# Optimization experiments

Measured on AMD Instinct MI355X. Metric: run time of the kernel, lower is better.

Reference implementation:

```python
import jax, jax.numpy as jnp
import numpy as np

N_NODES = 100000
N_EDGES = 1600000
IN_DIM = 128
OUT_DIM = 64
EDGE_DIM = 8


def setup_inputs() -> dict:
    key = jax.random.key(0)
    ks = jax.random.split(key, 7)
    h = jax.random.normal(ks[0], (N_NODES, IN_DIM), dtype=jnp.float32)
    edge_index = jax.random.randint(ks[1], (2, N_EDGES), 0, N_NODES, dtype=jnp.int64)
    edge_attr = jax.random.normal(ks[2], (N_EDGES, EDGE_DIM), dtype=jnp.float32)
    w_w = jax.random.normal(ks[3], (IN_DIM, OUT_DIM), dtype=jnp.float32) * (1.0 / np.sqrt(IN_DIM))
    w_b = jax.random.normal(ks[4], (OUT_DIM,), dtype=jnp.float32) * 0.01
    a_w = jax.random.normal(ks[5], (2 * OUT_DIM + EDGE_DIM, 1), dtype=jnp.float32) * 0.1
    a_b = jax.random.normal(ks[6], (1,), dtype=jnp.float32) * 0.01
    return {"h": h, "edge_index": edge_index, "edge_attr": edge_attr,
            "w_w": w_w, "w_b": w_b, "a_w": a_w, "a_b": a_b}


def reference(h, edge_index, edge_attr, w_w, w_b, a_w, a_b):
    n = h.shape[0]
    d = w_w.shape[1]
    wh = h @ w_w + w_b                              # [N, out_dim]
    row, col = edge_index[0], edge_index[1]
    # a([wh[row], wh[col], edge_attr]) == wh[row]@a1 + wh[col]@a2 + edge_attr@a3 + b
    a1, a2, a3 = a_w[:d], a_w[d:2 * d], a_w[2 * d:]
    s_row = wh @ a1                                 # [N, 1] per-node attention terms
    s_col = wh @ a2                                 # [N, 1]
    e = jax.nn.leaky_relu(s_row[row] + s_col[col] + edge_attr @ a3 + a_b)  # [E, 1]
    # segment softmax over edges grouped by destination `row`
    max_e = jax.ops.segment_max(e, row, num_segments=n)     # [N, 1]
    alpha = jnp.exp(e - max_e[row])                          # [E, 1]
    out = jax.ops.segment_sum(alpha * wh[col], row, num_segments=n)  # [N, out_dim]
    norm = jax.ops.segment_sum(alpha, row, num_segments=n)           # [N, 1]
    return out / (norm + 1e-8)
```

## Files before the change

kernel.cpp:

```cpp
#include <hip/hip_runtime.h>
#include <hip/hip_fp16.h>

#define IN_DIM 128
#define OUT_DIM 64
#define RPB 512
#define MAXB 200
#define EPB 2048

typedef __attribute__((ext_vector_type(8))) _Float16 half8;
typedef __attribute__((ext_vector_type(4))) float f32x4;

__global__ __launch_bounds__(256) void k_wh(
    const float* __restrict__ h, const float* __restrict__ w_w,
    const float* __restrict__ w_b, const float* __restrict__ a_w,
    __half* __restrict__ wh, float* __restrict__ s_row,
    float* __restrict__ s_col, int n_nodes) {
  __shared__ _Float16 wf[4 * 4 * 64 * 8];
  for (int idx = threadIdx.x; idx < IN_DIM * OUT_DIM; idx += 256) {
    int k = idx >> 6, c = idx & 63;
    int mt = c >> 4;
    int kt = k >> 5;
    int l = (((k >> 3) & 3) << 4) | (c & 15);
    int j = k & 7;
    wf[(((mt << 2) | kt) << 9) | (l << 3) | j] = (_Float16)w_w[idx];
  }
  __syncthreads();

  const int lane = threadIdx.x & 63;
  const int wv = threadIdx.x >> 6;

  half8 A[4][4];
#pragma unroll
  for (int mt = 0; mt < 4; ++mt)
#pragma unroll
    for (int kt = 0; kt < 4; ++kt)
      A[mt][kt] =
          *(const half8*)&wf[(((mt << 2) | kt) << 9) | (lane << 3)];

  const int cbase = (lane >> 4) << 2;
  f32x4 bq[4], a1q[4], a2q[4];
#pragma unroll
  for (int mt = 0; mt < 4; ++mt) {
    bq[mt] = *(const f32x4*)&w_b[mt * 16 + cbase];
    a1q[mt] = *(const f32x4*)&a_w[mt * 16 + cbase];
    a2q[mt] = *(const f32x4*)&a_w[OUT_DIM + mt * 16 + cbase];
  }

  const int ntiles = (n_nodes + 15) >> 4;
  const int tstride = gridDim.x << 2;
  for (int t = blockIdx.x * 4 + wv; t < ntiles; t += tstride) {
    const int n0 = t << 4;
    const int node = n0 + (lane & 15);
    const int nodec = node < n_nodes ? node : n_nodes - 1;
    const float4* hv =
        (const float4*)(h + (size_t)nodec * IN_DIM + ((lane >> 4) << 3));
    float4 p[8];
#pragma unroll
    for (int kt = 0; kt < 4; ++kt) {
      p[2 * kt] = hv[kt * 8];
      p[2 * kt + 1] = hv[kt * 8 + 1];
    }
    f32x4 C[4];
#pragma unroll
    for (int mt = 0; mt < 4; ++mt) C[mt] = (f32x4){0.f, 0.f, 0.f, 0.f};
#pragma unroll
    for (int kt = 0; kt < 4; ++kt) {
      const float4 u = p[2 * kt], v = p[2 * kt + 1];
      half8 B;
      B[0] = (_Float16)u.x; B[1] = (_Float16)u.y;
      B[2] = (_Float16)u.z; B[3] = (_Float16)u.w;
      B[4] = (_Float16)v.x; B[5] = (_Float16)v.y;
      B[6] = (_Float16)v.z; B[7] = (_Float16)v.w;
#pragma unroll
      for (int mt = 0; mt < 4; ++mt)
        C[mt] = __builtin_amdgcn_mfma_f32_16x16x32_f16(A[mt][kt], B, C[mt],
                                                       0, 0, 0);
    }
    float sr = 0.f, sc = 0.f;
    uint2 q[4];
#pragma unroll
    for (int mt = 0; mt < 4; ++mt) {
      f32x4 d = C[mt] + bq[mt];
      sr += d[0] * a1q[mt][0] + d[1] * a1q[mt][1] + d[2] * a1q[mt][2] +
            d[3] * a1q[mt][3];
      sc += d[0] * a2q[mt][0] + d[1] * a2q[mt][1] + d[2] * a2q[mt][2] +
            d[3] * a2q[mt][3];
      __half2 lo = __floats2half2_rn(d[0], d[1]);
      __half2 hi = __floats2half2_rn(d[2], d[3]);
      q[mt].x = *(unsigned int*)&lo;
      q[mt].y = *(unsigned int*)&hi;
    }
    if (node < n_nodes) {
      uint2* wrow = (uint2*)(wh + (size_t)node * OUT_DIM + cbase);
      wrow[0] = q[0];
      wrow[4] = q[1];
      wrow[8] = q[2];
      wrow[12] = q[3];
    }
    sr += __shfl_xor(sr, 16, 64);
    sr += __shfl_xor(sr, 32, 64);
    sc += __shfl_xor(sc, 16, 64);
    sc += __shfl_xor(sc, 32, 64);
    if (lane < 16 && node < n_nodes) {
      s_row[node] = sr;
      s_col[node] = sc;
    }
  }
}

__global__ __launch_bounds__(512) void k_pre(
    const int* __restrict__ ei, int* __restrict__ blockhist, int nedges) {
  __shared__ int hist[MAXB];
  for (int b = threadIdx.x; b < MAXB; b += 512) hist[b] = 0;
  __syncthreads();
  const int e0 = blockIdx.x * EPB;
  if (e0 + EPB <= nedges) {
    const int e = e0 + threadIdx.x;
    int r0 = ei[e];
    int r1 = ei[e + 512];
    int r2 = ei[e + 1024];
    int r3 = ei[e + 1536];
    atomicAdd(&hist[r0 >> 9], 1);
    atomicAdd(&hist[r1 >> 9], 1);
    atomicAdd(&hist[r2 >> 9], 1);
    atomicAdd(&hist[r3 >> 9], 1);
  } else {
#pragma unroll
    for (int r = 0; r < EPB / 512; ++r) {
      int e = e0 + r * 512 + threadIdx.x;
      if (e < nedges) atomicAdd(&hist[ei[e] >> 9], 1);
    }
  }
  __syncthreads();
  for (int b = threadIdx.x; b < MAXB; b += 512)
    blockhist[blockIdx.x * MAXB + b] = hist[b];
}

__global__ __launch_bounds__(512) void k_scanA(
    const int* __restrict__ blockhist, int* __restrict__ boff,
    int* __restrict__ cnt, int nbl) {
  __shared__ int sd[512];
  const int b = blockIdx.x, t = threadIdx.x;
  int i0 = 2 * t, i1 = 2 * t + 1;
  int v0 = (i0 < nbl) ? ((blockhist[i0 * MAXB + b] + 7) & ~7) : 0;
  int v1 = (i1 < nbl) ? ((blockhist[i1 * MAXB + b] + 7) & ~7) : 0;
  int ts = v0 + v1;
  sd[t] = ts;
  __syncthreads();
  for (int off = 1; off < 512; off <<= 1) {
    int x = (t >= off) ? sd[t - off] : 0;
    __syncthreads();
    sd[t] += x;
    __syncthreads();
  }
  int excl = sd[t] - ts;
  if (i0 < nbl) boff[i0 * MAXB + b] = excl;
  if (i1 < nbl) boff[i1 * MAXB + b] = excl + v0;
  if (t == 511) cnt[b] = sd[511];
}

__global__ __launch_bounds__(256) void k_scanB(
    const int* __restrict__ cnt, int* __restrict__ bbase, int nb) {
  __shared__ int sd[256];
  int t = threadIdx.x;
  int pc = (t < nb) ? ((cnt[t] + 15) & ~15) : 0;
  sd[t] = pc;
  __syncthreads();
  for (int off = 1; off < 256; off <<= 1) {
    int x = (t >= off) ? sd[t - off] : 0;
    __syncthreads();
    sd[t] += x;
    __syncthreads();
  }
  if (t < nb) bbase[t] = sd[t] - pc;
}

__global__ __launch_bounds__(512) void k_fill(
    const int* __restrict__ ei, const float* __restrict__ edge_attr,
    const float* __restrict__ a_w, const float* __restrict__ a_b,
    const float* __restrict__ s_row, const float* __restrict__ s_col,
    const int* __restrict__ boff, const int* __restrict__ bbase,
    int2* __restrict__ entA, int nedges, int nb) {
  __shared__ int cur[MAXB];
  for (int b = threadIdx.x; b < MAXB; b += 512)
    cur[b] = (b < nb) ? bbase[b] + boff[blockIdx.x * MAXB + b] : 0;
  float aw0 = a_w[128], aw1 = a_w[129], aw2 = a_w[130], aw3 = a_w[131];
  float aw4 = a_w[132], aw5 = a_w[133], aw6 = a_w[134], aw7 = a_w[135];
  float ab = a_b[0];
  __syncthreads();
  const int e0 = blockIdx.x * EPB;
  if (e0 + EPB <= nedges) {
    const int e = e0 + threadIdx.x;
    int row[4], col[4];
#pragma unroll
    for (int r = 0; r < 4; ++r) {
      row[r] = ei[e + r * 512];
      col[r] = ei[nedges + e + r * 512];
    }
    float4 u[4], v[4];
#pragma unroll
    for (int r = 0; r < 4; ++r) {
      const float4* ea = (const float4*)(edge_attr + (size_t)(e + r * 512) * 8);
      u[r] = ea[0];
      v[r] = ea[1];
    }
    float sr[4], sc[4];
#pragma unroll
    for (int r = 0; r < 4; ++r) {
      sr[r] = s_row[row[r]];
      sc[r] = s_col[col[r]];
    }
#pragma unroll
    for (int r = 0; r < 4; ++r) {
      float s = sr[r] + sc[r] + ab;
      s += u[r].x * aw0 + u[r].y * aw1 + u[r].z * aw2 + u[r].w * aw3;
      s += v[r].x * aw4 + v[r].y * aw5 + v[r].z * aw6 + v[r].w * aw7;
      float ev = (s > 0.f) ? s : 0.01f * s;
      float alpha = __expf(ev);
      int pos = atomicAdd(&cur[row[r] >> 9], 1);
      entA[pos] =
          make_int2(((row[r] & 511) << 17) | col[r], __float_as_int(alpha));
    }
  } else {
    for (int r = 0; r < EPB / 512; ++r) {
      int e = e0 + r * 512 + threadIdx.x;
      if (e < nedges) {
        int row = ei[e];
        int col = ei[nedges + e];
        const float4* ea = (const float4*)(edge_attr + (size_t)e * 8);
        float4 u = ea[0], v = ea[1];
        float s = s_row[row] + s_col[col] + ab;
        s += u.x * aw0 + u.y * aw1 + u.z * aw2 + u.w * aw3;
        s += v.x * aw4 + v.y * aw5 + v.z * aw6 + v.w * aw7;
        float ev = (s > 0.f) ? s : 0.01f * s;
        float alpha = __expf(ev);
        int pos = atomicAdd(&cur[row >> 9], 1);
        entA[pos] = make_int2(((row & 511) << 17) | col, __float_as_int(alpha));
      }
    }
  }
  __syncthreads();
  for (int b = threadIdx.x; b < nb; b += 512) {
    int c = cur[b], end = (c + 7) & ~7;
    for (int k = c; k < end; ++k) entA[k] = make_int2(-1, 0);
  }
}

__global__ __launch_bounds__(512) void k_sortb(
    const int2* __restrict__ entA, int2* __restrict__ entB,
    const int* __restrict__ cnt, const int* __restrict__ bbase,
    int* __restrict__ nodeoffs, int* __restrict__ nodecnt, int n_nodes) {
  __shared__ int hist[RPB];
  __shared__ int loffs[RPB];
  __shared__ int cur[RPB];
  const int b = blockIdx.x, t = threadIdx.x;
  const int c = cnt[b];
  const int base = bbase[b];
  const int row0 = b << 9;
  hist[t] = 0;
  __syncthreads();
  for (int i = t; i < c; i += 512) {
    int x = entA[base + i].x;
    if (x >= 0) atomicAdd(&hist[x >> 17], 1);
  }
  __syncthreads();
  int hh = hist[t];
  loffs[t] = hh;
  __syncthreads();
  for (int off = 1; off < 512; off <<= 1) {
    int x = (t >= off) ? loffs[t - off] : 0;
    __syncthreads();
    loffs[t] += x;
    __syncthreads();
  }
  int excl = loffs[t] - hh;
  cur[t] = excl;
  int node = row0 + t;
  if (node < n_nodes) {
    nodeoffs[node] = base + excl;
    nodecnt[node] = hh;
  }
  __syncthreads();
  for (int i = t; i < c; i += 512) {
    int2 p = entA[base + i];
    if (p.x >= 0) {
      int pos = atomicAdd(&cur[p.x >> 17], 1);
      entB[base + pos] = p;
    }
  }
}

__global__ __launch_bounds__(256) void k_agg(
    const int* __restrict__ nodeoffs, const int* __restrict__ nodecnt,
    const int2* __restrict__ ent, const __half* __restrict__ wh,
    float* __restrict__ out, int n_nodes) {
  int v = blockIdx.x * 4 + (threadIdx.x >> 6);
  if (v >= n_nodes) return;
  const int lane = threadIdx.x & 63;
  const int slot = lane >> 3, sub = lane & 7;
  const int start = __builtin_amdgcn_readfirstlane(nodeoffs[v]);
  const int deg = __builtin_amdgcn_readfirstlane(nodecnt[v]);
  const uint4* whq = (const uint4*)wh;
  float acc[8] = {0.f, 0.f, 0.f, 0.f, 0.f, 0.f, 0.f, 0.f};
  float l = 0.f;
  for (int base = 0; base < deg; base += 16) {
    const int i0 = base + slot, i1 = base + 8 + slot;
    const bool g0 = i0 < deg, g1 = i1 < deg;
    int2 p0 = make_int2(0, 0), p1 = make_int2(0, 0);
    if (g0) p0 = ent[start + i0];
    if (g1) p1 = ent[start + i1];
    uint4 q0 = make_uint4(0, 0, 0, 0), q1 = make_uint4(0, 0, 0, 0);
    if (g0) q0 = whq[(size_t)(p0.x & 0x1FFFF) * 8 + sub];
    if (g1) q1 = whq[(size_t)(p1.x & 0x1FFFF) * 8 + sub];
    if (g0) {
      float a = __int_as_float(p0.y);
      float2 f0 = __half22float2(*(__half2*)&q0.x);
      float2 f1 = __half22float2(*(__half2*)&q0.y);
      float2 f2 = __half22float2(*(__half2*)&q0.z);
      float2 f3 = __half22float2(*(__half2*)&q0.w);
      acc[0] = fmaf(a, f0.x, acc[0]); acc[1] = fmaf(a, f0.y, acc[1]);
      acc[2] = fmaf(a, f1.x, acc[2]); acc[3] = fmaf(a, f1.y, acc[3]);
      acc[4] = fmaf(a, f2.x, acc[4]); acc[5] = fmaf(a, f2.y, acc[5]);
      acc[6] = fmaf(a, f3.x, acc[6]); acc[7] = fmaf(a, f3.y, acc[7]);
      if (sub == 0) l += a;
    }
    if (g1) {
      float a = __int_as_float(p1.y);
      float2 f0 = __half22float2(*(__half2*)&q1.x);
      float2 f1 = __half22float2(*(__half2*)&q1.y);
      float2 f2 = __half22float2(*(__half2*)&q1.z);
      float2 f3 = __half22float2(*(__half2*)&q1.w);
      acc[0] = fmaf(a, f0.x, acc[0]); acc[1] = fmaf(a, f0.y, acc[1]);
      acc[2] = fmaf(a, f1.x, acc[2]); acc[3] = fmaf(a, f1.y, acc[3]);
      acc[4] = fmaf(a, f2.x, acc[4]); acc[5] = fmaf(a, f2.y, acc[5]);
      acc[6] = fmaf(a, f3.x, acc[6]); acc[7] = fmaf(a, f3.y, acc[7]);
      if (sub == 0) l += a;
    }
  }
#pragma unroll
  for (int c = 0; c < 8; ++c) {
    acc[c] += __shfl_xor(acc[c], 8, 64);
    acc[c] += __shfl_xor(acc[c], 16, 64);
    acc[c] += __shfl_xor(acc[c], 32, 64);
  }
  l += __shfl_xor(l, 8, 64);
  l += __shfl_xor(l, 16, 64);
  l += __shfl_xor(l, 32, 64);
  float lt = __shfl(l, 0, 64);
  if (slot == 0) {
    float inv = 1.0f / (lt + 1e-8f);
    float4 o0 = make_float4(acc[0] * inv, acc[1] * inv, acc[2] * inv,
                            acc[3] * inv);
    float4 o1 = make_float4(acc[4] * inv, acc[5] * inv, acc[6] * inv,
                            acc[7] * inv);
    float4* orow = (float4*)out + (size_t)v * 16 + sub * 2;
    orow[0] = o0;
    orow[1] = o1;
  }
}

extern "C" void kernel_launch(void* const* d_in, const int* in_sizes, int n_in,
                              void* d_out, int out_size, void* d_ws, size_t ws_size,
                              hipStream_t stream) {
  const float* h         = (const float*)d_in[0];
  const int*   ei        = (const int*)d_in[1];
  const float* edge_attr = (const float*)d_in[2];
  const float* w_w       = (const float*)d_in[3];
  const float* w_b       = (const float*)d_in[4];
  const float* a_w       = (const float*)d_in[5];
  const float* a_b       = (const float*)d_in[6];
  const int n_nodes = in_sizes[0] / IN_DIM;
  const int nedges  = in_sizes[1] / 2;
  const int nb   = (n_nodes + RPB - 1) / RPB;
  const int nebl = (nedges + EPB - 1) / EPB;

  const size_t entcap = (size_t)nedges + (size_t)nebl * nb * 8 + (size_t)nb * 16;

  __half* wh       = (__half*)d_ws;
  int2*  entA      = (int2*)(wh + (size_t)n_nodes * OUT_DIM);
  int*   cnt       = (int*)(entA + entcap);
  int*   bbase     = cnt + MAXB;
  int*   nodeoffs  = bbase + MAXB;
  int*   nodecnt   = nodeoffs + n_nodes;
  int2*  entB      = (int2*)(nodecnt + n_nodes);
  float* s_row     = (float*)entB;
  float* s_col     = s_row + n_nodes;
  int*   blockhist = (int*)(s_col + n_nodes);
  int*   boff      = blockhist + (size_t)nebl * MAXB;

  k_wh<<<640, 256, 0, stream>>>(h, w_w, w_b, a_w, wh, s_row, s_col, n_nodes);
  k_pre<<<nebl, 512, 0, stream>>>(ei, blockhist, nedges);
  k_scanA<<<nb, 512, 0, stream>>>(blockhist, boff, cnt, nebl);
  k_scanB<<<1, 256, 0, stream>>>(cnt, bbase, nb);
  k_fill<<<nebl, 512, 0, stream>>>(ei, edge_attr, a_w, a_b, s_row, s_col,
                                   boff, bbase, entA, nedges, nb);
  k_sortb<<<nb, 512, 0, stream>>>(entA, entB, cnt, bbase, nodeoffs, nodecnt, n_nodes);
  k_agg<<<(n_nodes + 3) / 4, 256, 0, stream>>>(nodeoffs, nodecnt, entB, wh,
                                               (float*)d_out, n_nodes);
}
```

Baseline: 272.9 us.

## Build CSR via global per-node atomic histogram instead of two-level bucket sort

Replaces the block-histogram bucket partition plus per-bucket local sort with a direct CSR build: per-node degree counting via global atomics, a three-stage device prefix scan, and per-edge atomic slot allocation in the fill kernel. This removes the k_sortb pass and the bucket padding, cutting an extra read/write of the edge array. In exchange it issues millions of global atomics to random addresses and makes edge order within each node nondeterministic. Node counters are zeroed inside the projection kernel.

Measured after the change: 371.4 us. 1.36x slower.

```diff
diff --git a/kernel.cpp b/kernel.cpp
--- a/kernel.cpp
+++ b/kernel.cpp
@@ -3,8 +3,6 @@
 
 #define IN_DIM 128
 #define OUT_DIM 64
-#define RPB 512
-#define MAXB 200
 #define EPB 2048
 
 typedef __attribute__((ext_vector_type(8))) _Float16 half8;
@@ -14,7 +12,11 @@
     const float* __restrict__ h, const float* __restrict__ w_w,
     const float* __restrict__ w_b, const float* __restrict__ a_w,
     __half* __restrict__ wh, float* __restrict__ s_row,
-    float* __restrict__ s_col, int n_nodes) {
+    float* __restrict__ s_col, int* __restrict__ nodecnt, int n_nodes) {
+  {
+    int tid = blockIdx.x * 256 + threadIdx.x;
+    if (tid < n_nodes) nodecnt[tid] = 0;
+  }
   __shared__ _Float16 wf[4 * 4 * 64 * 8];
   for (int idx = threadIdx.x; idx < IN_DIM * OUT_DIM; idx += 256) {
     int k = idx >> 6, c = idx & 63;
@@ -108,11 +110,8 @@
   }
 }
 
-__global__ __launch_bounds__(512) void k_pre(
-    const int* __restrict__ ei, int* __restrict__ blockhist, int nedges) {
-  __shared__ int hist[MAXB];
-  for (int b = threadIdx.x; b < MAXB; b += 512) hist[b] = 0;
-  __syncthreads();
+__global__ __launch_bounds__(512) void k_hist(
+    const int* __restrict__ ei, int* __restrict__ nodecnt, int nedges) {
   const int e0 = blockIdx.x * EPB;
   if (e0 + EPB <= nedges) {
     const int e = e0 + threadIdx.x;
@@ -120,74 +119,69 @@
     int r1 = ei[e + 512];
     int r2 = ei[e + 1024];
     int r3 = ei[e + 1536];
-    atomicAdd(&hist[r0 >> 9], 1);
-    atomicAdd(&hist[r1 >> 9], 1);
-    atomicAdd(&hist[r2 >> 9], 1);
-    atomicAdd(&hist[r3 >> 9], 1);
+    atomicAdd(&nodecnt[r0], 1);
+    atomicAdd(&nodecnt[r1], 1);
+    atomicAdd(&nodecnt[r2], 1);
+    atomicAdd(&nodecnt[r3], 1);
   } else {
 #pragma unroll
     for (int r = 0; r < EPB / 512; ++r) {
       int e = e0 + r * 512 + threadIdx.x;
-      if (e < nedges) atomicAdd(&hist[ei[e] >> 9], 1);
-    }
-  }
+      if (e < nedges) atomicAdd(&nodecnt[ei[e]], 1);
+    }
+  }
+}
+
+__global__ __launch_bounds__(1024) void k_scan1(
+    const int* __restrict__ nodecnt, int* __restrict__ nodeoffs,
+    int* __restrict__ blocksum, int n_nodes) {
+  __shared__ int sd[1024];
+  const int t = threadIdx.x;
+  const int i = blockIdx.x * 1024 + t;
+  int v = (i < n_nodes) ? nodecnt[i] : 0;
+  sd[t] = v;
   __syncthreads();
-  for (int b = threadIdx.x; b < MAXB; b += 512)
-    blockhist[blockIdx.x * MAXB + b] = hist[b];
-}
-
-__global__ __launch_bounds__(512) void k_scanA(
-    const int* __restrict__ blockhist, int* __restrict__ boff,
-    int* __restrict__ cnt, int nbl) {
-  __shared__ int sd[512];
-  const int b = blockIdx.x, t = threadIdx.x;
-  int i0 = 2 * t, i1 = 2 * t + 1;
-  int v0 = (i0 < nbl) ? ((blockhist[i0 * MAXB + b] + 7) & ~7) : 0;
-  int v1 = (i1 < nbl) ? ((blockhist[i1 * MAXB + b] + 7) & ~7) : 0;
-  int ts = v0 + v1;
-  sd[t] = ts;
-  __syncthreads();
-  for (int off = 1; off < 512; off <<= 1) {
+  for (int off = 1; off < 1024; off <<= 1) {
     int x = (t >= off) ? sd[t - off] : 0;
     __syncthreads();
     sd[t] += x;
     __syncthreads();
   }
-  int excl = sd[t] - ts;
-  if (i0 < nbl) boff[i0 * MAXB + b] = excl;
-  if (i1 < nbl) boff[i1 * MAXB + b] = excl + v0;
-  if (t == 511) cnt[b] = sd[511];
-}
-
-__global__ __launch_bounds__(256) void k_scanB(
-    const int* __restrict__ cnt, int* __restrict__ bbase, int nb) {
-  __shared__ int sd[256];
-  int t = threadIdx.x;
-  int pc = (t < nb) ? ((cnt[t] + 15) & ~15) : 0;
-  sd[t] = pc;
+  if (i < n_nodes) nodeoffs[i] = sd[t] - v;
+  if (t == 1023) blocksum[blockIdx.x] = sd[1023];
+}
+
+__global__ __launch_bounds__(128) void k_scan2(
+    const int* __restrict__ blocksum, int* __restrict__ blockbase, int nsb) {
+  __shared__ int sd[128];
+  const int t = threadIdx.x;
+  int v = (t < nsb) ? blocksum[t] : 0;
+  sd[t] = v;
   __syncthreads();
-  for (int off = 1; off < 256; off <<= 1) {
+  for (int off = 1; off < 128; off <<= 1) {
     int x = (t >= off) ? sd[t - off] : 0;
     __syncthreads();
     sd[t] += x;
     __syncthreads();
   }
-  if (t < nb) bbase[t] = sd[t] - pc;
+  if (t < nsb) blockbase[t] = sd[t] - v;
+}
+
+__global__ __launch_bounds__(1024) void k_scan3(
+    int* __restrict__ nodeoffs, const int* __restrict__ blockbase,
+    int n_nodes) {
+  const int i = blockIdx.x * 1024 + threadIdx.x;
+  if (i < n_nodes) nodeoffs[i] += blockbase[blockIdx.x];
 }
 
 __global__ __launch_bounds__(512) void k_fill(
     const int* __restrict__ ei, const float* __restrict__ edge_attr,
     const float* __restrict__ a_w, const float* __restrict__ a_b,
     const float* __restrict__ s_row, const float* __restrict__ s_col,
-    const int* __restrict__ boff, const int* __restrict__ bbase,
-    int2* __restrict__ entA, int nedges, int nb) {
-  __shared__ int cur[MAXB];
-  for (int b = threadIdx.x; b < MAXB; b += 512)
-    cur[b] = (b < nb) ? bbase[b] + boff[blockIdx.x * MAXB + b] : 0;
+    int* __restrict__ nodeoffs, int2* __restrict__ ent, int nedges) {
   float aw0 = a_w[128], aw1 = a_w[129], aw2 = a_w[130], aw3 = a_w[131];
   float aw4 = a_w[132], aw5 = a_w[133], aw6 = a_w[134], aw7 = a_w[135];
   float ab = a_b[0];
-  __syncthreads();
   const int e0 = blockIdx.x * EPB;
   if (e0 + EPB <= nedges) {
     const int e = e0 + threadIdx.x;
@@ -197,6 +191,9 @@
       row[r] = ei[e + r * 512];
       col[r] = ei[nedges + e + r * 512];
     }
+    int pos[4];
+#pragma unroll
+    for (int r = 0; r < 4; ++r) pos[r] = atomicAdd(&nodeoffs[row[r]], 1);
     float4 u[4], v[4];
 #pragma unroll
     for (int r = 0; r < 4; ++r) {
@@ -217,9 +214,7 @@
       s += v[r].x * aw4 + v[r].y * aw5 + v[r].z * aw6 + v[r].w * aw7;
       float ev = (s > 0.f) ? s : 0.01f * s;
       float alpha = __expf(ev);
-      int pos = atomicAdd(&cur[row[r] >> 9], 1);
-      entA[pos] =
-          make_int2(((row[r] & 511) << 17) | col[r], __float_as_int(alpha));
+      ent[pos[r]] = make_int2(col[r], __float_as_int(alpha));
     }
   } else {
     for (int r = 0; r < EPB / 512; ++r) {
@@ -227,6 +222,7 @@
       if (e < nedges) {
         int row = ei[e];
         int col = ei[nedges + e];
+        int pos = atomicAdd(&nodeoffs[row], 1);
         const float4* ea = (const float4*)(edge_attr + (size_t)e * 8);
         float4 u = ea[0], v = ea[1];
         float s = s_row[row] + s_col[col] + ab;
@@ -234,58 +230,8 @@
         s += v.x * aw4 + v.y * aw5 + v.z * aw6 + v.w * aw7;
         float ev = (s > 0.f) ? s : 0.01f * s;
         float alpha = __expf(ev);
-        int pos = atomicAdd(&cur[row >> 9], 1);
-        entA[pos] = make_int2(((row & 511) << 17) | col, __float_as_int(alpha));
+        ent[pos] = make_int2(col, __float_as_int(alpha));
       }
-    }
-  }
-  __syncthreads();
-  for (int b = threadIdx.x; b < nb; b += 512) {
-    int c = cur[b], end = (c + 7) & ~7;
-    for (int k = c; k < end; ++k) entA[k] = make_int2(-1, 0);
-  }
-}
-
-__global__ __launch_bounds__(512) void k_sortb(
-    const int2* __restrict__ entA, int2* __restrict__ entB,
-    const int* __restrict__ cnt, const int* __restrict__ bbase,
-    int* __restrict__ nodeoffs, int* __restrict__ nodecnt, int n_nodes) {
-  __shared__ int hist[RPB];
-  __shared__ int loffs[RPB];
-  __shared__ int cur[RPB];
-  const int b = blockIdx.x, t = threadIdx.x;
-  const int c = cnt[b];
-  const int base = bbase[b];
-  const int row0 = b << 9;
-  hist[t] = 0;
-  __syncthreads();
-  for (int i = t; i < c; i += 512) {
-    int x = entA[base + i].x;
-    if (x >= 0) atomicAdd(&hist[x >> 17], 1);
-  }
-  __syncthreads();
-  int hh = hist[t];
-  loffs[t] = hh;
-  __syncthreads();
-  for (int off = 1; off < 512; off <<= 1) {
-    int x = (t >= off) ? loffs[t - off] : 0;
-    __syncthreads();
-    loffs[t] += x;
-    __syncthreads();
-  }
-  int excl = loffs[t] - hh;
-  cur[t] = excl;
-  int node = row0 + t;
-  if (node < n_nodes) {
-    nodeoffs[node] = base + excl;
-    nodecnt[node] = hh;
-  }
-  __syncthreads();
-  for (int i = t; i < c; i += 512) {
-    int2 p = entA[base + i];
-    if (p.x >= 0) {
-      int pos = atomicAdd(&cur[p.x >> 17], 1);
-      entB[base + pos] = p;
     }
   }
 }
@@ -298,8 +244,9 @@
   if (v >= n_nodes) return;
   const int lane = threadIdx.x & 63;
   const int slot = lane >> 3, sub = lane & 7;
-  const int start = __builtin_amdgcn_readfirstlane(nodeoffs[v]);
+  const int endp = __builtin_amdgcn_readfirstlane(nodeoffs[v]);
   const int deg = __builtin_amdgcn_readfirstlane(nodecnt[v]);
+  const int start = endp - deg;
   const uint4* whq = (const uint4*)wh;
   float acc[8] = {0.f, 0.f, 0.f, 0.f, 0.f, 0.f, 0.f, 0.f};
   float l = 0.f;
@@ -310,8 +257,8 @@
     if (g0) p0 = ent[start + i0];
     if (g1) p1 = ent[start + i1];
     uint4 q0 = make_uint4(0, 0, 0, 0), q1 = make_uint4(0, 0, 0, 0);
-    if (g0) q0 = whq[(size_t)(p0.x & 0x1FFFF) * 8 + sub];
-    if (g1) q1 = whq[(size_t)(p1.x & 0x1FFFF) * 8 + sub];
+    if (g0) q0 = whq[(size_t)p0.x * 8 + sub];
+    if (g1) q1 = whq[(size_t)p1.x * 8 + sub];
     if (g0) {
       float a = __int_as_float(p0.y);
       float2 f0 = __half22float2(*(__half2*)&q0.x);
@@ -371,30 +318,26 @@
   const float* a_b       = (const float*)d_in[6];
   const int n_nodes = in_sizes[0] / IN_DIM;
   const int nedges  = in_sizes[1] / 2;
-  const int nb   = (n_nodes + RPB - 1) / RPB;
   const int nebl = (nedges + EPB - 1) / EPB;
-
-  const size_t entcap = (size_t)nedges + (size_t)nebl * nb * 8 + (size_t)nb * 16;
+  const int nsb  = (n_nodes + 1023) / 1024;
 
   __half* wh       = (__half*)d_ws;
-  int2*  entA      = (int2*)(wh + (size_t)n_nodes * OUT_DIM);
-  int*   cnt       = (int*)(entA + entcap);
-  int*   bbase     = cnt + MAXB;
-  int*   nodeoffs  = bbase + MAXB;
-  int*   nodecnt   = nodeoffs + n_nodes;
-  int2*  entB      = (int2*)(nodecnt + n_nodes);
-  float* s_row     = (float*)entB;
+  int2*  ent       = (int2*)(wh + (size_t)n_nodes * OUT_DIM);
+  int*   nodecnt   = (int*)(ent + (size_t)nedges);
+  int*   nodeoffs  = nodecnt + n_nodes;
+  int*   blocksum  = nodeoffs + n_nodes;
+  int*   blockbase = blocksum + 128;
+  float* s_row     = (float*)(blockbase + 128);
   float* s_col     = s_row + n_nodes;
-  int*   blockhist = (int*)(s_col + n_nodes);
-  int*   boff      = blockhist + (size_t)nebl * MAXB;
-
-  k_wh<<<640, 256, 0, stream>>>(h, w_w, w_b, a_w, wh, s_row, s_col, n_nodes);
-  k_pre<<<nebl, 512, 0, stream>>>(ei, blockhist, nedges);
-  k_scanA<<<nb, 512, 0, stream>>>(blockhist, boff, cnt, nebl);
-  k_scanB<<<1, 256, 0, stream>>>(cnt, bbase, nb);
+
+  k_wh<<<640, 256, 0, stream>>>(h, w_w, w_b, a_w, wh, s_row, s_col,
+                                nodecnt, n_nodes);
+  k_hist<<<nebl, 512, 0, stream>>>(ei, nodecnt, nedges);
+  k_scan1<<<nsb, 1024, 0, stream>>>(nodecnt, nodeoffs, blocksum, n_nodes);
+  k_scan2<<<1, 128, 0, stream>>>(blocksum, blockbase, nsb);
+  k_scan3<<<nsb, 1024, 0, stream>>>(nodeoffs, blockbase, n_nodes);
   k_fill<<<nebl, 512, 0, stream>>>(ei, edge_attr, a_w, a_b, s_row, s_col,
-                                   boff, bbase, entA, nedges, nb);
-  k_sortb<<<nb, 512, 0, stream>>>(entA, entB, cnt, bbase, nodeoffs, nodecnt, n_nodes);
-  k_agg<<<(n_nodes + 3) / 4, 256, 0, stream>>>(nodeoffs, nodecnt, entB, wh,
+                                   nodeoffs, ent, nedges);
+  k_agg<<<(n_nodes + 3) / 4, 256, 0, stream>>>(nodeoffs, nodecnt, ent, wh,
                                                (float*)d_out, n_nodes);
 }
```

## Defer attention score and exp into aggregation, dropping s_col and random gathers

Applied to the files above, without the earlier changes.

k_fill no longer gathers s_row/s_col per edge or computes leaky-relu and exp. It stores only the edge_attr dot product. k_agg recomputes wh[col]·a2 from the fp16 wh row it already loads, using an 8-lane shuffle reduction, then adds s_row[v] and a_b and applies leaky-relu and exp. This removes two random gathers per edge and the s_col buffer, at the cost of extra shuffles and FMAs in the aggregation loop. s_col is now computed from fp16-rounded wh, which slightly changes precision.

New measurement: 258.3 us. 1.06x faster.

```diff
diff --git a/kernel.cpp b/kernel.cpp
--- a/kernel.cpp
+++ b/kernel.cpp
@@ -13,8 +13,7 @@
 __global__ __launch_bounds__(256) void k_wh(
     const float* __restrict__ h, const float* __restrict__ w_w,
     const float* __restrict__ w_b, const float* __restrict__ a_w,
-    __half* __restrict__ wh, float* __restrict__ s_row,
-    float* __restrict__ s_col, int n_nodes) {
+    __half* __restrict__ wh, float* __restrict__ s_row, int n_nodes) {
   __shared__ _Float16 wf[4 * 4 * 64 * 8];
   for (int idx = threadIdx.x; idx < IN_DIM * OUT_DIM; idx += 256) {
     int k = idx >> 6, c = idx & 63;
@@ -38,12 +37,11 @@
           *(const half8*)&wf[(((mt << 2) | kt) << 9) | (lane << 3)];
 
   const int cbase = (lane >> 4) << 2;
-  f32x4 bq[4], a1q[4], a2q[4];
+  f32x4 bq[4], a1q[4];
 #pragma unroll
   for (int mt = 0; mt < 4; ++mt) {
     bq[mt] = *(const f32x4*)&w_b[mt * 16 + cbase];
     a1q[mt] = *(const f32x4*)&a_w[mt * 16 + cbase];
-    a2q[mt] = *(const f32x4*)&a_w[OUT_DIM + mt * 16 + cbase];
   }
 
   const int ntiles = (n_nodes + 15) >> 4;
@@ -76,15 +74,13 @@
         C[mt] = __builtin_amdgcn_mfma_f32_16x16x32_f16(A[mt][kt], B, C[mt],
                                                        0, 0, 0);
     }
-    float sr = 0.f, sc = 0.f;
+    float sr = 0.f;
     uint2 q[4];
 #pragma unroll
     for (int mt = 0; mt < 4; ++mt) {
       f32x4 d = C[mt] + bq[mt];
       sr += d[0] * a1q[mt][0] + d[1] * a1q[mt][1] + d[2] * a1q[mt][2] +
             d[3] * a1q[mt][3];
-      sc += d[0] * a2q[mt][0] + d[1] * a2q[mt][1] + d[2] * a2q[mt][2] +
-            d[3] * a2q[mt][3];
       __half2 lo = __floats2half2_rn(d[0], d[1]);
       __half2 hi = __floats2half2_rn(d[2], d[3]);
       q[mt].x = *(unsigned int*)&lo;
@@ -99,11 +95,8 @@
     }
     sr += __shfl_xor(sr, 16, 64);
     sr += __shfl_xor(sr, 32, 64);
-    sc += __shfl_xor(sc, 16, 64);
-    sc += __shfl_xor(sc, 32, 64);
     if (lane < 16 && node < n_nodes) {
       s_row[node] = sr;
-      s_col[node] = sc;
     }
   }
 }
@@ -177,8 +170,7 @@
 
 __global__ __launch_bounds__(512) void k_fill(
     const int* __restrict__ ei, const float* __restrict__ edge_attr,
-    const float* __restrict__ a_w, const float* __restrict__ a_b,
-    const float* __restrict__ s_row, const float* __restrict__ s_col,
+    const float* __restrict__ a_w,
     const int* __restrict__ boff, const int* __restrict__ bbase,
     int2* __restrict__ entA, int nedges, int nb) {
   __shared__ int cur[MAXB];
@@ -186,7 +178,6 @@
     cur[b] = (b < nb) ? bbase[b] + boff[blockIdx.x * MAXB + b] : 0;
   float aw0 = a_w[128], aw1 = a_w[129], aw2 = a_w[130], aw3 = a_w[131];
   float aw4 = a_w[132], aw5 = a_w[133], aw6 = a_w[134], aw7 = a_w[135];
-  float ab = a_b[0];
   __syncthreads();
   const int e0 = blockIdx.x * EPB;
   if (e0 + EPB <= nedges) {
@@ -204,22 +195,13 @@
       u[r] = ea[0];
       v[r] = ea[1];
     }
-    float sr[4], sc[4];
 #pragma unroll
     for (int r = 0; r < 4; ++r) {
-      sr[r] = s_row[row[r]];
-      sc[r] = s_col[col[r]];
-    }
-#pragma unroll
-    for (int r = 0; r < 4; ++r) {
-      float s = sr[r] + sc[r] + ab;
-      s += u[r].x * aw0 + u[r].y * aw1 + u[r].z * aw2 + u[r].w * aw3;
+      float s = u[r].x * aw0 + u[r].y * aw1 + u[r].z * aw2 + u[r].w * aw3;
       s += v[r].x * aw4 + v[r].y * aw5 + v[r].z * aw6 + v[r].w * aw7;
-      float ev = (s > 0.f) ? s : 0.01f * s;
-      float alpha = __expf(ev);
       int pos = atomicAdd(&cur[row[r] >> 9], 1);
       entA[pos] =
-          make_int2(((row[r] & 511) << 17) | col[r], __float_as_int(alpha));
+          make_int2(((row[r] & 511) << 17) | col[r], __float_as_int(s));
     }
   } else {
     for (int r = 0; r < EPB / 512; ++r) {
@@ -229,13 +211,10 @@
         int col = ei[nedges + e];
         const float4* ea = (const float4*)(edge_attr + (size_t)e * 8);
         float4 u = ea[0], v = ea[1];
-        float s = s_row[row] + s_col[col] + ab;
-        s += u.x * aw0 + u.y * aw1 + u.z * aw2 + u.w * aw3;
+        float s = u.x * aw0 + u.y * aw1 + u.z * aw2 + u.w * aw3;
         s += v.x * aw4 + v.y * aw5 + v.z * aw6 + v.w * aw7;
-        float ev = (s > 0.f) ? s : 0.01f * s;
-        float alpha = __expf(ev);
         int pos = atomicAdd(&cur[row >> 9], 1);
-        entA[pos] = make_int2(((row & 511) << 17) | col, __float_as_int(alpha));
+        entA[pos] = make_int2(((row & 511) << 17) | col, __float_as_int(s));
       }
     }
   }
@@ -293,13 +272,17 @@
 __global__ __launch_bounds__(256) void k_agg(
     const int* __restrict__ nodeoffs, const int* __restrict__ nodecnt,
     const int2* __restrict__ ent, const __half* __restrict__ wh,
-    float* __restrict__ out, int n_nodes) {
+    const float* __restrict__ s_row, const float* __restrict__ a_w,
+    const float* __restrict__ a_b, float* __restrict__ out, int n_nodes) {
   int v = blockIdx.x * 4 + (threadIdx.x >> 6);
   if (v >= n_nodes) return;
   const int lane = threadIdx.x & 63;
   const int slot = lane >> 3, sub = lane & 7;
   const int start = __builtin_amdgcn_readfirstlane(nodeoffs[v]);
   const int deg = __builtin_amdgcn_readfirstlane(nodecnt[v]);
+  const float sab = s_row[v] + a_b[0];
+  const float4* a2p = (const float4*)(a_w + OUT_DIM + sub * 8);
+  const float4 a2lo = a2p[0], a2hi = a2p[1];
   const uint4* whq = (const uint4*)wh;
   float acc[8] = {0.f, 0.f, 0.f, 0.f, 0.f, 0.f, 0.f, 0.f};
   float l = 0.f;
@@ -313,11 +296,19 @@
     if (g0) q0 = whq[(size_t)(p0.x & 0x1FFFF) * 8 + sub];
     if (g1) q1 = whq[(size_t)(p1.x & 0x1FFFF) * 8 + sub];
     if (g0) {
-      float a = __int_as_float(p0.y);
       float2 f0 = __half22float2(*(__half2*)&q0.x);
       float2 f1 = __half22float2(*(__half2*)&q0.y);
       float2 f2 = __half22float2(*(__half2*)&q0.z);
       float2 f3 = __half22float2(*(__half2*)&q0.w);
+      float d = f0.x * a2lo.x + f0.y * a2lo.y + f1.x * a2lo.z +
+                f1.y * a2lo.w + f2.x * a2hi.x + f2.y * a2hi.y +
+                f3.x * a2hi.z + f3.y * a2hi.w;
+      d += __shfl_xor(d, 1, 64);
+      d += __shfl_xor(d, 2, 64);
+      d += __shfl_xor(d, 4, 64);
+      float s = sab + __int_as_float(p0.y) + d;
+      float ev = (s > 0.f) ? s : 0.01f * s;
+      float a = __expf(ev);
       acc[0] = fmaf(a, f0.x, acc[0]); acc[1] = fmaf(a, f0.y, acc[1]);
       acc[2] = fmaf(a, f1.x, acc[2]); acc[3] = fmaf(a, f1.y, acc[3]);
       acc[4] = fmaf(a, f2.x, acc[4]); acc[5] = fmaf(a, f2.y, acc[5]);
@@ -325,11 +316,19 @@
       if (sub == 0) l += a;
     }
     if (g1) {
-      float a = __int_as_float(p1.y);
       float2 f0 = __half22float2(*(__half2*)&q1.x);
       float2 f1 = __half22float2(*(__half2*)&q1.y);
       float2 f2 = __half22float2(*(__half2*)&q1.z);
       float2 f3 = __half22float2(*(__half2*)&q1.w);
+      float d = f0.x * a2lo.x + f0.y * a2lo.y + f1.x * a2lo.z +
+                f1.y * a2lo.w + f2.x * a2hi.x + f2.y * a2hi.y +
+                f3.x * a2hi.z + f3.y * a2hi.w;
+      d += __shfl_xor(d, 1, 64);
+      d += __shfl_xor(d, 2, 64);
+      d += __shfl_xor(d, 4, 64);
+      float s = sab + __int_as_float(p1.y) + d;
+      float ev = (s > 0.f) ? s : 0.01f * s;
+      float a = __expf(ev);
       acc[0] = fmaf(a, f0.x, acc[0]); acc[1] = fmaf(a, f0.y, acc[1]);
       acc[2] = fmaf(a, f1.x, acc[2]); acc[3] = fmaf(a, f1.y, acc[3]);
       acc[4] = fmaf(a, f2.x, acc[4]); acc[5] = fmaf(a, f2.y, acc[5]);
@@ -382,19 +381,20 @@
   int*   bbase     = cnt + MAXB;
   int*   nodeoffs  = bbase + MAXB;
   int*   nodecnt   = nodeoffs + n_nodes;
-  int2*  entB      = (int2*)(nodecnt + n_nodes);
-  float* s_row     = (float*)entB;
-  float* s_col     = s_row + n_nodes;
-  int*   blockhist = (int*)(s_col + n_nodes);
+  float* s_row     = (float*)(nodecnt + n_nodes);
+  int2*  entB      = (int2*)(s_row + n_nodes);
+  int*   blockhist = (int*)entB;
   int*   boff      = blockhist + (size_t)nebl * MAXB;
 
-  k_wh<<<640, 256, 0, stream>>>(h, w_w, w_b, a_w, wh, s_row, s_col, n_nodes);
+  k_wh<<<640, 256, 0, stream>>>(h, w_w, w_b, a_w, wh, s_row, n_nodes);
   k_pre<<<nebl, 512, 0, stream>>>(ei, blockhist, nedges);
   k_scanA<<<nb, 512, 0, stream>>>(blockhist, boff, cnt, nebl);
   k_scanB<<<1, 256, 0, stream>>>(cnt, bbase, nb);
-  k_fill<<<nebl, 512, 0, stream>>>(ei, edge_attr, a_w, a_b, s_row, s_col,
-                                   boff, bbase, entA, nedges, nb);
-  k_sortb<<<nb, 512, 0, stream>>>(entA, entB, cnt, bbase, nodeoffs, nodecnt, n_nodes);
+  k_fill<<<nebl, 512, 0, stream>>>(ei, edge_attr, a_w, boff, bbase, entA,
+                                   nedges, nb);
+  k_sortb<<<nb, 512, 0, stream>>>(entA, entB, cnt, bbase, nodeoffs, nodecnt,
+                                  n_nodes);
   k_agg<<<(n_nodes + 3) / 4, 256, 0, stream>>>(nodeoffs, nodecnt, entB, wh,
+                                               s_row, a_w, a_b,
                                                (float*)d_out, n_nodes);
 }
```

## Replace per-node sort and aggregation with bucket-level LDS atomic accumulation

Applied to the files above, without the earlier changes.

Drops the second counting-sort pass (k_sortb) and the per-node gather kernel. A new k_edge kernel has one 1024-thread block per 256-row bucket, which reads the bucket's unsorted entries once and accumulates alpha*wh[col] and the normaliser with shared-memory float atomics, using a rotated column layout to spread LDS banks. The attention score is now finished in k_edge (s_row + s_col + bias, leaky_relu, exp), so k_fill only stores the edge_attr dot product. Buckets shrink from 512 to 256 rows to fit a 64KB LDS accumulator. This trades one global read/write pass for heavy LDS atomic traffic, lower occupancy and possible load imbalance across buckets.

After: 888.5 us. 3.26x slower.

```diff
diff --git a/kernel.cpp b/kernel.cpp
--- a/kernel.cpp
+++ b/kernel.cpp
@@ -3,8 +3,8 @@
 
 #define IN_DIM 128
 #define OUT_DIM 64
-#define RPB 512
-#define MAXB 200
+#define RPB 256
+#define MAXB 400
 #define EPB 2048
 
 typedef __attribute__((ext_vector_type(8))) _Float16 half8;
@@ -120,15 +120,15 @@
     int r1 = ei[e + 512];
     int r2 = ei[e + 1024];
     int r3 = ei[e + 1536];
-    atomicAdd(&hist[r0 >> 9], 1);
-    atomicAdd(&hist[r1 >> 9], 1);
-    atomicAdd(&hist[r2 >> 9], 1);
-    atomicAdd(&hist[r3 >> 9], 1);
+    atomicAdd(&hist[r0 >> 8], 1);
+    atomicAdd(&hist[r1 >> 8], 1);
+    atomicAdd(&hist[r2 >> 8], 1);
+    atomicAdd(&hist[r3 >> 8], 1);
   } else {
 #pragma unroll
     for (int r = 0; r < EPB / 512; ++r) {
       int e = e0 + r * 512 + threadIdx.x;
-      if (e < nedges) atomicAdd(&hist[ei[e] >> 9], 1);
+      if (e < nedges) atomicAdd(&hist[ei[e] >> 8], 1);
     }
   }
   __syncthreads();
@@ -159,14 +159,14 @@
   if (t == 511) cnt[b] = sd[511];
 }
 
-__global__ __launch_bounds__(256) void k_scanB(
+__global__ __launch_bounds__(512) void k_scanB(
     const int* __restrict__ cnt, int* __restrict__ bbase, int nb) {
-  __shared__ int sd[256];
+  __shared__ int sd[512];
   int t = threadIdx.x;
   int pc = (t < nb) ? ((cnt[t] + 15) & ~15) : 0;
   sd[t] = pc;
   __syncthreads();
-  for (int off = 1; off < 256; off <<= 1) {
+  for (int off = 1; off < 512; off <<= 1) {
     int x = (t >= off) ? sd[t - off] : 0;
     __syncthreads();
     sd[t] += x;
@@ -177,8 +177,7 @@
 
 __global__ __launch_bounds__(512) void k_fill(
     const int* __restrict__ ei, const float* __restrict__ edge_attr,
-    const float* __restrict__ a_w, const float* __restrict__ a_b,
-    const float* __restrict__ s_row, const float* __restrict__ s_col,
+    const float* __restrict__ a_w,
     const int* __restrict__ boff, const int* __restrict__ bbase,
     int2* __restrict__ entA, int nedges, int nb) {
   __shared__ int cur[MAXB];
@@ -186,7 +185,6 @@
     cur[b] = (b < nb) ? bbase[b] + boff[blockIdx.x * MAXB + b] : 0;
   float aw0 = a_w[128], aw1 = a_w[129], aw2 = a_w[130], aw3 = a_w[131];
   float aw4 = a_w[132], aw5 = a_w[133], aw6 = a_w[134], aw7 = a_w[135];
-  float ab = a_b[0];
   __syncthreads();
   const int e0 = blockIdx.x * EPB;
   if (e0 + EPB <= nedges) {
@@ -204,22 +202,13 @@
       u[r] = ea[0];
       v[r] = ea[1];
     }
-    float sr[4], sc[4];
 #pragma unroll
     for (int r = 0; r < 4; ++r) {
-      sr[r] = s_row[row[r]];
-      sc[r] = s_col[col[r]];
-    }
-#pragma unroll
-    for (int r = 0; r < 4; ++r) {
-      float s = sr[r] + sc[r] + ab;
-      s += u[r].x * aw0 + u[r].y * aw1 + u[r].z * aw2 + u[r].w * aw3;
+      float s = u[r].x * aw0 + u[r].y * aw1 + u[r].z * aw2 + u[r].w * aw3;
       s += v[r].x * aw4 + v[r].y * aw5 + v[r].z * aw6 + v[r].w * aw7;
-      float ev = (s > 0.f) ? s : 0.01f * s;
-      float alpha = __expf(ev);
-      int pos = atomicAdd(&cur[row[r] >> 9], 1);
+      int pos = atomicAdd(&cur[row[r] >> 8], 1);
       entA[pos] =
-          make_int2(((row[r] & 511) << 17) | col[r], __float_as_int(alpha));
+          make_int2(((row[r] & 255) << 17) | col[r], __float_as_int(s));
     }
   } else {
     for (int r = 0; r < EPB / 512; ++r) {
@@ -229,13 +218,10 @@
         int col = ei[nedges + e];
         const float4* ea = (const float4*)(edge_attr + (size_t)e * 8);
         float4 u = ea[0], v = ea[1];
-        float s = s_row[row] + s_col[col] + ab;
-        s += u.x * aw0 + u.y * aw1 + u.z * aw2 + u.w * aw3;
+        float s = u.x * aw0 + u.y * aw1 + u.z * aw2 + u.w * aw3;
         s += v.x * aw4 + v.y * aw5 + v.z * aw6 + v.w * aw7;
-        float ev = (s > 0.f) ? s : 0.01f * s;
-        float alpha = __expf(ev);
-        int pos = atomicAdd(&cur[row >> 9], 1);
-        entA[pos] = make_int2(((row & 511) << 17) | col, __float_as_int(alpha));
+        int pos = atomicAdd(&cur[row >> 8], 1);
+        entA[pos] = make_int2(((row & 255) << 17) | col, __float_as_int(s));
       }
     }
   }
@@ -246,116 +232,96 @@
   }
 }
 
-__global__ __launch_bounds__(512) void k_sortb(
-    const int2* __restrict__ entA, int2* __restrict__ entB,
-    const int* __restrict__ cnt, const int* __restrict__ bbase,
-    int* __restrict__ nodeoffs, int* __restrict__ nodecnt, int n_nodes) {
-  __shared__ int hist[RPB];
-  __shared__ int loffs[RPB];
-  __shared__ int cur[RPB];
-  const int b = blockIdx.x, t = threadIdx.x;
-  const int c = cnt[b];
-  const int base = bbase[b];
-  const int row0 = b << 9;
-  hist[t] = 0;
-  __syncthreads();
-  for (int i = t; i < c; i += 512) {
-    int x = entA[base + i].x;
-    if (x >= 0) atomicAdd(&hist[x >> 17], 1);
-  }
-  __syncthreads();
-  int hh = hist[t];
-  loffs[t] = hh;
-  __syncthreads();
-  for (int off = 1; off < 512; off <<= 1) {
-    int x = (t >= off) ? loffs[t - off] : 0;
-    __syncthreads();
-    loffs[t] += x;
-    __syncthreads();
-  }
-  int excl = loffs[t] - hh;
-  cur[t] = excl;
-  int node = row0 + t;
-  if (node < n_nodes) {
-    nodeoffs[node] = base + excl;
-    nodecnt[node] = hh;
-  }
-  __syncthreads();
-  for (int i = t; i < c; i += 512) {
-    int2 p = entA[base + i];
-    if (p.x >= 0) {
-      int pos = atomicAdd(&cur[p.x >> 17], 1);
-      entB[base + pos] = p;
-    }
-  }
-}
-
-__global__ __launch_bounds__(256) void k_agg(
-    const int* __restrict__ nodeoffs, const int* __restrict__ nodecnt,
-    const int2* __restrict__ ent, const __half* __restrict__ wh,
-    float* __restrict__ out, int n_nodes) {
-  int v = blockIdx.x * 4 + (threadIdx.x >> 6);
-  if (v >= n_nodes) return;
-  const int lane = threadIdx.x & 63;
-  const int slot = lane >> 3, sub = lane & 7;
-  const int start = __builtin_amdgcn_readfirstlane(nodeoffs[v]);
-  const int deg = __builtin_amdgcn_readfirstlane(nodecnt[v]);
+__global__ __launch_bounds__(1024) void k_edge(
+    const int2* __restrict__ entA, const int* __restrict__ cnt,
+    const int* __restrict__ bbase, const __half* __restrict__ wh,
+    const float* __restrict__ s_row, const float* __restrict__ s_col,
+    const float* __restrict__ a_b, float* __restrict__ out, int n_nodes) {
+  __shared__ float acc[RPB * 64];
+  __shared__ float nrm[RPB];
+  __shared__ float sr[RPB];
+  const int b = blockIdx.x;
+  const int row0 = b << 8;
+  const int t = threadIdx.x;
+  for (int i = t; i < RPB * 64; i += 1024) acc[i] = 0.f;
+  if (t < RPB) {
+    nrm[t] = 0.f;
+    int node = row0 + t;
+    sr[t] = (node < n_nodes) ? s_row[node] : 0.f;
+  }
+  __syncthreads();
+  const int c = __builtin_amdgcn_readfirstlane(cnt[b]);
+  const int base = __builtin_amdgcn_readfirstlane(bbase[b]);
+  const float ab = a_b[0];
+  const int slot = t >> 3;
+  const int sub = t & 7;
   const uint4* whq = (const uint4*)wh;
-  float acc[8] = {0.f, 0.f, 0.f, 0.f, 0.f, 0.f, 0.f, 0.f};
-  float l = 0.f;
-  for (int base = 0; base < deg; base += 16) {
-    const int i0 = base + slot, i1 = base + 8 + slot;
-    const bool g0 = i0 < deg, g1 = i1 < deg;
-    int2 p0 = make_int2(0, 0), p1 = make_int2(0, 0);
-    if (g0) p0 = ent[start + i0];
-    if (g1) p1 = ent[start + i1];
+  for (int i = slot; i < c; i += 256) {
+    const int i1 = i + 128;
+    int2 p0 = entA[base + i];
+    int2 p1 = (i1 < c) ? entA[base + i1] : make_int2(-1, 0);
+    const bool g0 = p0.x >= 0, g1 = p1.x >= 0;
+    int col0 = p0.x & 0x1FFFF, col1 = p1.x & 0x1FFFF;
     uint4 q0 = make_uint4(0, 0, 0, 0), q1 = make_uint4(0, 0, 0, 0);
-    if (g0) q0 = whq[(size_t)(p0.x & 0x1FFFF) * 8 + sub];
-    if (g1) q1 = whq[(size_t)(p1.x & 0x1FFFF) * 8 + sub];
+    float sc0 = 0.f, sc1 = 0.f;
+    if (g0) { q0 = whq[(size_t)col0 * 8 + sub]; sc0 = s_col[col0]; }
+    if (g1) { q1 = whq[(size_t)col1 * 8 + sub]; sc1 = s_col[col1]; }
     if (g0) {
-      float a = __int_as_float(p0.y);
+      int rl = p0.x >> 17;
+      float s = sr[rl] + sc0 + __int_as_float(p0.y) + ab;
+      float ev = (s > 0.f) ? s : 0.01f * s;
+      float a = __expf(ev);
       float2 f0 = __half22float2(*(__half2*)&q0.x);
       float2 f1 = __half22float2(*(__half2*)&q0.y);
       float2 f2 = __half22float2(*(__half2*)&q0.z);
       float2 f3 = __half22float2(*(__half2*)&q0.w);
-      acc[0] = fmaf(a, f0.x, acc[0]); acc[1] = fmaf(a, f0.y, acc[1]);
-      acc[2] = fmaf(a, f1.x, acc[2]); acc[3] = fmaf(a, f1.y, acc[3]);
-      acc[4] = fmaf(a, f2.x, acc[4]); acc[5] = fmaf(a, f2.y, acc[5]);
-      acc[6] = fmaf(a, f3.x, acc[6]); acc[7] = fmaf(a, f3.y, acc[7]);
-      if (sub == 0) l += a;
+      const int rb = rl << 6, rot = (rl & 3) << 3, d = sub << 3;
+      atomicAdd(&acc[rb + ((d + 0 + rot) & 63)], a * f0.x);
+      atomicAdd(&acc[rb + ((d + 1 + rot) & 63)], a * f0.y);
+      atomicAdd(&acc[rb + ((d + 2 + rot) & 63)], a * f1.x);
+      atomicAdd(&acc[rb + ((d + 3 + rot) & 63)], a * f1.y);
+      atomicAdd(&acc[rb + ((d + 4 + rot) & 63)], a * f2.x);
+      atomicAdd(&acc[rb + ((d + 5 + rot) & 63)], a * f2.y);
+      atomicAdd(&acc[rb + ((d + 6 + rot) & 63)], a * f3.x);
+      atomicAdd(&acc[rb + ((d + 7 + rot) & 63)], a * f3.y);
+      if (sub == 0) atomicAdd(&nrm[rl], a);
     }
     if (g1) {
-      float a = __int_as_float(p1.y);
+      int rl = p1.x >> 17;
+      float s = sr[rl] + sc1 + __int_as_float(p1.y) + ab;
+      float ev = (s > 0.f) ? s : 0.01f * s;
+      float a = __expf(ev);
       float2 f0 = __half22float2(*(__half2*)&q1.x);
       float2 f1 = __half22float2(*(__half2*)&q1.y);
       float2 f2 = __half22float2(*(__half2*)&q1.z);
       float2 f3 = __half22float2(*(__half2*)&q1.w);
-      acc[0] = fmaf(a, f0.x, acc[0]); acc[1] = fmaf(a, f0.y, acc[1]);
-      acc[2] = fmaf(a, f1.x, acc[2]); acc[3] = fmaf(a, f1.y, acc[3]);
-      acc[4] = fmaf(a, f2.x, acc[4]); acc[5] = fmaf(a, f2.y, acc[5]);
-      acc[6] = fmaf(a, f3.x, acc[6]); acc[7] = fmaf(a, f3.y, acc[7]);
-      if (sub == 0) l += a;
-    }
-  }
-#pragma unroll
-  for (int c = 0; c < 8; ++c) {
-    acc[c] += __shfl_xor(acc[c], 8, 64);
-    acc[c] += __shfl_xor(acc[c], 16, 64);
-    acc[c] += __shfl_xor(acc[c], 32, 64);
-  }
-  l += __shfl_xor(l, 8, 64);
-  l += __shfl_xor(l, 16, 64);
-  l += __shfl_xor(l, 32, 64);
-  float lt = __shfl(l, 0, 64);
-  if (slot == 0) {
-    float inv = 1.0f / (lt + 1e-8f);
-    float4 o0 = make_float4(acc[0] * inv, acc[1] * inv, acc[2] * inv,
-                            acc[3] * inv);
-    float4 o1 = make_float4(acc[4] * inv, acc[5] * inv, acc[6] * inv,
-                            acc[7] * inv);
-    float4* orow = (float4*)out + (size_t)v * 16 + sub * 2;
-    orow[0] = o0;
-    orow[1] = o1;
+      const int rb = rl << 6, rot = (rl & 3) << 3, d = sub << 3;
+      atomicAdd(&acc[rb + ((d + 0 + rot) & 63)], a * f0.x);
+      atomicAdd(&acc[rb + ((d + 1 + rot) & 63)], a * f0.y);
+      atomicAdd(&acc[rb + ((d + 2 + rot) & 63)], a * f1.x);
+      atomicAdd(&acc[rb + ((d + 3 + rot) & 63)], a * f1.y);
+      atomicAdd(&acc[rb + ((d + 4 + rot) & 63)], a * f2.x);
+      atomicAdd(&acc[rb + ((d + 5 + rot) & 63)], a * f2.y);
+      atomicAdd(&acc[rb + ((d + 6 + rot) & 63)], a * f3.x);
+      atomicAdd(&acc[rb + ((d + 7 + rot) & 63)], a * f3.y);
+      if (sub == 0) atomicAdd(&nrm[rl], a);
+    }
+  }
+  __syncthreads();
+  for (int idx = t; idx < RPB * 16; idx += 1024) {
+    const int row = idx >> 4;
+    const int node = row0 + row;
+    if (node < n_nodes) {
+      const int d0 = (idx & 15) << 2;
+      const int rb = row << 6, rot = (row & 3) << 3;
+      const float inv = 1.0f / (nrm[row] + 1e-8f);
+      float4 o;
+      o.x = acc[rb + ((d0 + 0 + rot) & 63)] * inv;
+      o.y = acc[rb + ((d0 + 1 + rot) & 63)] * inv;
+      o.z = acc[rb + ((d0 + 2 + rot) & 63)] * inv;
+      o.w = acc[rb + ((d0 + 3 + rot) & 63)] * inv;
+      ((float4*)out)[(size_t)node * 16 + (idx & 15)] = o;
+    }
   }
 }
 
@@ -380,10 +346,7 @@
   int2*  entA      = (int2*)(wh + (size_t)n_nodes * OUT_DIM);
   int*   cnt       = (int*)(entA + entcap);
   int*   bbase     = cnt + MAXB;
-  int*   nodeoffs  = bbase + MAXB;
-  int*   nodecnt   = nodeoffs + n_nodes;
-  int2*  entB      = (int2*)(nodecnt + n_nodes);
-  float* s_row     = (float*)entB;
+  float* s_row     = (float*)(bbase + MAXB);
   float* s_col     = s_row + n_nodes;
   int*   blockhist = (int*)(s_col + n_nodes);
   int*   boff      = blockhist + (size_t)nebl * MAXB;
@@ -391,10 +354,9 @@
   k_wh<<<640, 256, 0, stream>>>(h, w_w, w_b, a_w, wh, s_row, s_col, n_nodes);
   k_pre<<<nebl, 512, 0, stream>>>(ei, blockhist, nedges);
   k_scanA<<<nb, 512, 0, stream>>>(blockhist, boff, cnt, nebl);
-  k_scanB<<<1, 256, 0, stream>>>(cnt, bbase, nb);
-  k_fill<<<nebl, 512, 0, stream>>>(ei, edge_attr, a_w, a_b, s_row, s_col,
-                                   boff, bbase, entA, nedges, nb);
-  k_sortb<<<nb, 512, 0, stream>>>(entA, entB, cnt, bbase, nodeoffs, nodecnt, n_nodes);
-  k_agg<<<(n_nodes + 3) / 4, 256, 0, stream>>>(nodeoffs, nodecnt, entB, wh,
-                                               (float*)d_out, n_nodes);
-}
+  k_scanB<<<1, 512, 0, stream>>>(cnt, bbase, nb);
+  k_fill<<<nebl, 512, 0, stream>>>(ei, edge_attr, a_w, boff, bbase, entA,
+                                   nedges, nb);
+  k_edge<<<nb, 1024, 0, stream>>>(entA, cnt, bbase, wh, s_row, s_col, a_b,
+                                  (float*)d_out, n_nodes);
+}
```
